# Kernel optimization log

Measured on AMD Instinct MI355X. Metric: run time of the kernel, lower is better.

Reference implementation:

```python
import jax, jax.numpy as jnp
import numpy as np

HEADS = 8
DK = 64   # key_size (defaults to size_per_head)
DV = 64   # size_per_head
RATE = 4
OUT = HEADS * DV  # 512


def extract_seq_patches(x, kernel, rate):
    # x: [b, L, d] -> [b, L, kernel, d]; strided local window gather
    b, L, d = x.shape
    k_size = kernel + (rate - 1) * (kernel - 1)
    p_right = (k_size - 1) // 2
    p_left = k_size - 1 - p_right
    xp = jnp.pad(x, ((0, 0), (p_left, p_right), (0, 0)))
    patches = [xp[:, i:i + L] for i in range(0, k_size, rate)]  # kernel slices
    return jnp.stack(patches, axis=2)


def setup_inputs() -> dict:
    key = jax.random.key(0)
    k1, k2, k3, k4 = jax.random.split(key, 4)
    s = 1.0 / np.sqrt(OUT)
    x = jax.random.normal(k1, (2, 4096, OUT), dtype=jnp.float32)
    Wq = jax.random.normal(k2, (OUT, HEADS * DK), dtype=jnp.float32) * s
    Wk = jax.random.normal(k3, (OUT, HEADS * DK), dtype=jnp.float32) * s
    Wv = jax.random.normal(k4, (OUT, HEADS * DV), dtype=jnp.float32) * s
    return {"x": x, "Wq": Wq, "Wk": Wk, "Wv": Wv}


def reference(x, Wq, Wk, Wv):
    b, L, d = x.shape
    pad = RATE - L % RATE  # torch code always pads (pad=RATE when L % RATE == 0)
    xpad = jnp.pad(x, ((0, 0), (0, pad), (0, 0)))
    nL = L + pad
    n = nL // RATE
    kernel = 2 * RATE - 1  # 1 + 2*neighbors

    qw = xpad @ Wq
    kw = xpad @ Wk
    vw = xpad @ Wv

    kwp = extract_seq_patches(kw, kernel, RATE)  # [b, nL, K, H*dk]
    vwp = extract_seq_patches(vw, kernel, RATE)  # [b, nL, K, H*dv]

    # [b, h, r, n, d]
    qw = qw.reshape(b, n, RATE, HEADS, DK).transpose(0, 3, 2, 1, 4)
    kw = kw.reshape(b, n, RATE, HEADS, DK).transpose(0, 3, 2, 1, 4)
    vw = vw.reshape(b, n, RATE, HEADS, DV).transpose(0, 3, 2, 1, 4)
    # [b, h, r, n, K, d]
    kwp = kwp.reshape(b, n, RATE, kernel, HEADS, DK).transpose(0, 4, 2, 1, 3, 5)
    vwp = vwp.reshape(b, n, RATE, kernel, HEADS, DV).transpose(0, 4, 2, 1, 3, 5)

    scale = 1.0 / np.sqrt(DK)
    a = jnp.einsum('bhrnd,bhrmd->bhrnm', qw, kw) * scale    # strided scores [b,h,r,n,n]
    ap = jnp.einsum('bhrnd,bhrnkd->bhrnk', qw, kwp) * scale  # local scores  [b,h,r,n,K]

    A = jax.nn.softmax(jnp.concatenate([a, ap], axis=-1), axis=-1)
    a, ap = A[..., :n], A[..., n:]

    o = jnp.einsum('bhrnm,bhrmd->bhrnd', a, vw) + jnp.einsum('bhrnk,bhrnkd->bhrnd', ap, vwp)
    o = o.transpose(0, 3, 2, 1, 4).reshape(b, nL, HEADS * DV)
    return o[:, :L]
```

## Files before the change

### kernel.cpp

```cpp
#include <hip/hip_runtime.h>
#include <hip/hip_bf16.h>


#define BATCH 2
#define LSEQ  4096
#define DMODEL 512
#define NH    8
#define DHEAD 64
#define NPAD  1088
#define QSCALE 0.18033688011112042f

typedef __bf16 bf16x8 __attribute__((ext_vector_type(8)));
typedef __attribute__((ext_vector_type(4))) float f32x4;
typedef unsigned short u16;
typedef unsigned int u32;
typedef __attribute__((ext_vector_type(8))) u16 u16x8;
typedef __attribute__((ext_vector_type(4))) u16 u16x4;

__device__ __forceinline__ u16 f2bf(float f) {
    u32 u = __float_as_uint(f);
    u += 0x7fffu + ((u >> 16) & 1u);
    return (u16)(u >> 16);
}

__device__ __forceinline__ void gload16(const u16* g, u16* l) {
    __builtin_amdgcn_global_load_lds(
        (const __attribute__((address_space(1))) u32*)(const void*)g,
        (__attribute__((address_space(3))) u32*)(void*)l, 16, 0, 0);
}

__global__ __launch_bounds__(256) void prep_kernel(
    const float* __restrict__ x,
    const float* __restrict__ Wq, const float* __restrict__ Wk, const float* __restrict__ Wv,
    u16* __restrict__ xb, u16* __restrict__ Wt,
    u16* __restrict__ Kb, u16* __restrict__ Vb)
{
    const int bid = blockIdx.x, tid = threadIdx.x;
    if (bid < 2048) {
        const size_t i0 = (size_t)bid * 2048 + (size_t)tid * 8;
        float4 a = *(const float4*)(x + i0);
        float4 b = *(const float4*)(x + i0 + 4);
        u16x8 o = { f2bf(a.x), f2bf(a.y), f2bf(a.z), f2bf(a.w),
                    f2bf(b.x), f2bf(b.y), f2bf(b.z), f2bf(b.w) };
        *(u16x8*)(xb + i0) = o;
    } else if (bid < 2240) {
        const int wb  = bid - 2048;
        const int mat = wb >> 6;
        const int t   = wb & 63;
        const int k0  = (t >> 3) * 64, c0 = (t & 7) * 64;
        const float* W = (mat == 0) ? Wq : (mat == 1) ? Wk : Wv;
        __shared__ u16 Ws[64][72];
        #pragma unroll
        for (int i = 0; i < 4; ++i) {
            const int chunk = i * 256 + tid;
            const int kr = chunk >> 4, c4 = (chunk & 15) * 4;
            float4 v = *(const float4*)(W + (size_t)(k0 + kr) * DMODEL + c0 + c4);
            u16x4 q = { f2bf(v.x), f2bf(v.y), f2bf(v.z), f2bf(v.w) };
            *(u16x4*)&Ws[kr][c4] = q;
        }
        __syncthreads();
        const int cc = tid >> 2, kq = (tid & 3) * 16;
        alignas(16) u16 tmp[16];
        #pragma unroll
        for (int kk = 0; kk < 16; ++kk) tmp[kk] = Ws[kq + kk][cc];
        u16* dst = Wt + (size_t)(mat * 512 + c0 + cc) * DMODEL + k0 + kq;
        *(u16x8*)dst       = *(const u16x8*)&tmp[0];
        *(u16x8*)(dst + 8) = *(const u16x8*)&tmp[8];
    } else {
        const int g = bid - 2240;
        const u16x8 z = {0,0,0,0,0,0,0,0};
        u16* kt = Kb + ((size_t)g * NPAD + 1024) * DHEAD + tid * 16;
        *(u16x8*)kt       = z;
        *(u16x8*)(kt + 8) = z;
        u16* vt = Vb + ((size_t)g * DHEAD + (tid >> 2)) * NPAD + 1024 + (tid & 3) * 16;
        *(u16x8*)vt       = z;
        *(u16x8*)(vt + 8) = z;
    }
}

__global__ __launch_bounds__(256) void gemm_kernel(
    const u16* __restrict__ xb, const u16* __restrict__ Wt,
    u16* __restrict__ Qb, u16* __restrict__ Kb, u16* __restrict__ Vb)
{
    const int m0 = blockIdx.x * 128;
    const int nt = blockIdx.y;
    const int n0 = nt * 128;
    const int tid = threadIdx.x;
    const int w = tid >> 6, l = tid & 63, lr = l & 15, lh = l >> 4;
    const int wr = w >> 1, wc = w & 1;

    __shared__ u16 smem[16896];
    u16* As = smem;
    u16* Bs = smem + 8192;

    f32x4 acc[4][4];
    const f32x4 fzero = {0.f, 0.f, 0.f, 0.f};
    #pragma unroll
    for (int mi = 0; mi < 4; ++mi)
        #pragma unroll
        for (int nj = 0; nj < 4; ++nj) acc[mi][nj] = fzero;

    for (int kt = 0; kt < 8; ++kt) {
        const int k0 = kt * 64;
        #pragma unroll
        for (int i = 0; i < 4; ++i) {
            const int cid = i * 256 + tid;
            const int row = cid >> 3, ch = cid & 7;
            const int sch = ch ^ (row & 7);
            u16* dstA = As + (i * 256 + w * 64) * 8;
            u16* dstB = Bs + (i * 256 + w * 64) * 8;
            gload16(xb + (size_t)(m0 + row) * DMODEL + k0 + sch * 8, dstA);
            gload16(Wt + (size_t)(n0 + row) * DMODEL + k0 + sch * 8, dstB);
        }
        __syncthreads();

        #pragma unroll
        for (int kk = 0; kk < 2; ++kk) {
            const int cs = (kk * 4 + lh) ^ (lr & 7);
            bf16x8 af[4], bfr[4];
            #pragma unroll
            for (int mi = 0; mi < 4; ++mi)
                af[mi] = *(const bf16x8*)(As + (wr * 64 + mi * 16 + lr) * 64 + cs * 8);
            #pragma unroll
            for (int nj = 0; nj < 4; ++nj)
                bfr[nj] = *(const bf16x8*)(Bs + (wc * 64 + nj * 16 + lr) * 64 + cs * 8);
            #pragma unroll
            for (int mi = 0; mi < 4; ++mi)
                #pragma unroll
                for (int nj = 0; nj < 4; ++nj)
                    acc[mi][nj] = __builtin_amdgcn_mfma_f32_16x16x32_bf16(af[mi], bfr[nj], acc[mi][nj], 0, 0, 0);
        }
        __syncthreads();
    }

    const int mat = nt >> 2;
    const int hp  = nt & 3;
    if (mat < 2) {
        u16* Ob = (mat == 0) ? Qb : Kb;
        const float osc = (mat == 0) ? QSCALE : 1.0f;
        #pragma unroll
        for (int mi = 0; mi < 4; ++mi) {
            const int gmb = m0 + wr * 64 + mi * 16 + lh * 4;
            const int b = gmb >> 12;
            #pragma unroll
            for (int rr = 0; rr < 4; ++rr) {
                const int t = (gmb + rr) & 4095;
                const int n = t >> 2, r = t & 3;
                #pragma unroll
                for (int nj = 0; nj < 4; ++nj) {
                    const int c  = wc * 64 + nj * 16 + lr;
                    const int h  = hp * 2 + (c >> 6);
                    const int dk = c & 63;
                    const size_t g = ((size_t)(b * NH + h)) * 4 + r;
                    Ob[(g * NPAD + n) * DHEAD + dk] = f2bf(acc[mi][nj][rr] * osc);
                }
            }
        }
    } else {
        #pragma unroll
        for (int mi = 0; mi < 4; ++mi) {
            const int nrel = wr * 16 + mi * 4 + lh;
            #pragma unroll
            for (int nj = 0; nj < 4; ++nj) {
                const int c = wc * 64 + nj * 16 + lr;
                #pragma unroll
                for (int rr = 0; rr < 4; ++rr)
                    smem[c * 132 + rr * 32 + nrel] = f2bf(acc[mi][nj][rr]);
            }
        }
        __syncthreads();
        const int b  = m0 >> 12;
        const int nb = (m0 & 4095) >> 2;
        #pragma unroll
        for (int e = 0; e < 2; ++e) {
            const int chunk = e * 256 + tid;
            const int c = chunk & 127, r = chunk >> 7;
            const int h  = hp * 2 + (c >> 6);
            const int dv = c & 63;
            const size_t g = ((size_t)(b * NH + h)) * 4 + r;
            u16* dst = Vb + (g * DHEAD + dv) * NPAD + nb;
            const u16* src = smem + c * 132 + r * 32;
            alignas(16) u16 tmp[32];
            #pragma unroll
            for (int q8 = 0; q8 < 8; ++q8)
                *(u16x4*)&tmp[q8 * 4] = *(const u16x4*)(src + q8 * 4);
            #pragma unroll
            for (int q16 = 0; q16 < 4; ++q16)
                *(u16x8*)(dst + q16 * 8) = *(const u16x8*)&tmp[q16 * 8];
        }
    }
}

__global__ __launch_bounds__(512) void attn_kernel(
    const u16* __restrict__ Qb, const u16* __restrict__ Kb, const u16* __restrict__ Vb,
    float* __restrict__ out)
{
    const int g  = blockIdx.x;
    const int b  = g >> 5;
    const int h  = (g >> 2) & 7;
    const int r  = g & 3;
    const int q0 = blockIdx.y * 128;
    const int tid = threadIdx.x;
    const int w  = tid >> 6;
    const int l  = tid & 63;
    const int lr = l & 15, lh = l >> 4;

    const u16* Qg  = Qb + (size_t)g * NPAD * DHEAD;
    const u16* Kg  = Kb + (size_t)g * NPAD * DHEAD;
    const u16* Vtg = Vb + (size_t)g * DHEAD * NPAD;

    __shared__ u16 KV[2][2][4096];
    __shared__ u16 Ps[8][16][68];

    const int srow = tid >> 3;
    const int ssch = (tid & 7) ^ (srow & 7);
    const u16* ksrc0 = Kg  + (size_t)srow * DHEAD + ssch * 8;
    const u16* vsrc0 = Vtg + (size_t)srow * NPAD  + ssch * 8;

    bf16x8 qa[2];
    {
        const u16* qrow = Qg + (size_t)(q0 + w * 16 + lr) * DHEAD;
        qa[0] = *(const bf16x8*)(qrow + lh * 8);
        qa[1] = *(const bf16x8*)(qrow + 32 + lh * 8);
    }

    const f32x4 fzero = {0.f, 0.f, 0.f, 0.f};
    f32x4 o[4];
    #pragma unroll
    for (int j = 0; j < 4; ++j) o[j] = fzero;
    float Lpart[4] = {0.f, 0.f, 0.f, 0.f};

    const int qw0 = q0 + w * 16;

    gload16(ksrc0, &KV[0][0][w * 512]);
    gload16(vsrc0 + 0, &KV[0][1][w * 512]);

    int cur = 0;
    for (int mt = 0; mt < 17; ++mt) {
        if (mt < 16) {
            gload16(ksrc0 + (size_t)(mt + 1) * 4096, &KV[cur ^ 1][0][w * 512]);
            gload16(vsrc0 + (mt + 1) * 64,           &KV[cur ^ 1][1][w * 512]);
            asm volatile("s_waitcnt vmcnt(2)" ::: "memory");
        } else {
            asm volatile("s_waitcnt vmcnt(0)" ::: "memory");
        }
        __builtin_amdgcn_s_barrier();

        const u16* Kbuf = KV[cur][0];
        const u16* Vbuf = KV[cur][1];

        f32x4 s[4];
        #pragma unroll
        for (int ni = 0; ni < 4; ++ni) {
            s[ni] = fzero;
            #pragma unroll
            for (int kk = 0; kk < 2; ++kk) {
                const int slot = (kk * 4 + lh) ^ (lr & 7);
                bf16x8 kb = *(const bf16x8*)(Kbuf + ((ni * 16 + lr) * 8 + slot) * 8);
                s[ni] = __builtin_amdgcn_mfma_f32_16x16x32_bf16(qa[kk], kb, s[ni], 0, 0, 0);
            }
        }

        const int m0 = mt * 64;
        const bool special = (mt == 16) || ((m0 + 66 >= qw0) && (m0 <= qw0 + 18));
        if (!special) {
            #pragma unroll
            for (int ni = 0; ni < 4; ++ni) {
                #pragma unroll
                for (int rr = 0; rr < 4; ++rr) {
                    const float p = __builtin_amdgcn_exp2f(s[ni][rr]);
                    Lpart[rr] += p;
                    Ps[w][lh * 4 + rr][ni * 16 + lr] = f2bf(p);
                }
            }
        } else {
            #pragma unroll
            for (int ni = 0; ni < 4; ++ni) {
                const int mg = m0 + ni * 16 + lr;
                #pragma unroll
                for (int rr = 0; rr < 4; ++rr) {
                    const int qg = qw0 + lh * 4 + rr;
                    float v = s[ni][rr];
                    const int dd = mg - qg;
                    if (mg > 1024)                 v = -1e30f;
                    else if (dd >= -3 && dd <= 3)  v += 1.0f;
                    const float p = __builtin_amdgcn_exp2f(v);
                    Lpart[rr] += p;
                    Ps[w][lh * 4 + rr][ni * 16 + lr] = f2bf(p);
                }
            }
        }

        #pragma unroll
        for (int kk = 0; kk < 2; ++kk) {
            bf16x8 pa = *(const bf16x8*)&Ps[w][lr][kk * 32 + lh * 8];
            #pragma unroll
            for (int j = 0; j < 4; ++j) {
                const int slot = (kk * 4 + lh) ^ (lr & 7);
                bf16x8 vb = *(const bf16x8*)(Vbuf + ((j * 16 + lr) * 8 + slot) * 8);
                o[j] = __builtin_amdgcn_mfma_f32_16x16x32_bf16(pa, vb, o[j], 0, 0, 0);
            }
        }
        __syncthreads();
        cur ^= 1;
    }

    #pragma unroll
    for (int rr = 0; rr < 4; ++rr) {
        float s_ = Lpart[rr];
        #pragma unroll
        for (int off = 1; off < 16; off <<= 1)
            s_ += __shfl_xor(s_, off, 16);
        const int qg = qw0 + lh * 4 + rr;
        const int coob = (qg < 3 ? 3 - qg : 0) + (qg > 1021 ? qg - 1021 : 0);
        const float inv = 1.0f / (s_ + (float)coob);
        const int t = qg * 4 + r;
        float* orow = out + ((size_t)b * LSEQ + t) * DMODEL + h * DHEAD;
        #pragma unroll
        for (int j = 0; j < 4; ++j)
            orow[j * 16 + lr] = o[j][rr] * inv;
    }
}

extern "C" void kernel_launch(void* const* d_in, const int* in_sizes, int n_in,
                              void* d_out, int out_size, void* d_ws, size_t ws_size,
                              hipStream_t stream) {
    const float* x  = (const float*)d_in[0];
    const float* Wq = (const float*)d_in[1];
    const float* Wk = (const float*)d_in[2];
    const float* Wv = (const float*)d_in[3];
    float* out = (float*)d_out;

    const size_t SZ = (size_t)BATCH * NH * 4 * NPAD * DHEAD;
    u16* Qb = (u16*)d_ws;
    u16* Kb = Qb + SZ;
    u16* Vb = Kb + SZ;

    u16* xb = (u16*)d_out;
    u16* Wt = xb + (size_t)8192 * 512;

    prep_kernel<<<2304, 256, 0, stream>>>(x, Wq, Wk, Wv, xb, Wt, Kb, Vb);

    dim3 gg(64, 12);
    gemm_kernel<<<gg, 256, 0, stream>>>(xb, Wt, Qb, Kb, Vb);

    dim3 ga(64, 8);
    attn_kernel<<<ga, 512, 0, stream>>>(Qb, Kb, Vb, out);
}
```

Baseline: 67.91 us.

## Double query rows per wave, drop padded key tile, reuse K/V fragments

Each attention wave now handles 32 query rows instead of 16, so every K and V fragment read from shared memory feeds two MFMAs and the grid is halved. The 17th key tile covering padded positions is dropped. Its contribution is folded analytically into the softmax denominator, which removes the zero-fill pass for padding in the prep kernel. It also adds s_setprio around the MFMA phases and uses the hardware bf16 conversion. The risks are fewer blocks available for occupancy, more register pressure, and a fragile analytic correction for the padding rows.

```diff
diff --git a/kernel.cpp b/kernel.cpp
--- a/kernel.cpp
+++ b/kernel.cpp
@@ -23,6 +23,11 @@
     return (u16)(u >> 16);
 }
 
+__device__ __forceinline__ u16 cvt_bf(float f) {
+    __bf16 t = (__bf16)f;
+    return *(const u16*)&t;
+}
+
 __device__ __forceinline__ void gload16(const u16* g, u16* l) {
     __builtin_amdgcn_global_load_lds(
         (const __attribute__((address_space(1))) u32*)(const void*)g,
@@ -32,8 +37,7 @@
 __global__ __launch_bounds__(256) void prep_kernel(
     const float* __restrict__ x,
     const float* __restrict__ Wq, const float* __restrict__ Wk, const float* __restrict__ Wv,
-    u16* __restrict__ xb, u16* __restrict__ Wt,
-    u16* __restrict__ Kb, u16* __restrict__ Vb)
+    u16* __restrict__ xb, u16* __restrict__ Wt)
 {
     const int bid = blockIdx.x, tid = threadIdx.x;
     if (bid < 2048) {
@@ -43,7 +47,7 @@
         u16x8 o = { f2bf(a.x), f2bf(a.y), f2bf(a.z), f2bf(a.w),
                     f2bf(b.x), f2bf(b.y), f2bf(b.z), f2bf(b.w) };
         *(u16x8*)(xb + i0) = o;
-    } else if (bid < 2240) {
+    } else {
         const int wb  = bid - 2048;
         const int mat = wb >> 6;
         const int t   = wb & 63;
@@ -66,15 +70,6 @@
         u16* dst = Wt + (size_t)(mat * 512 + c0 + cc) * DMODEL + k0 + kq;
         *(u16x8*)dst       = *(const u16x8*)&tmp[0];
         *(u16x8*)(dst + 8) = *(const u16x8*)&tmp[8];
-    } else {
-        const int g = bid - 2240;
-        const u16x8 z = {0,0,0,0,0,0,0,0};
-        u16* kt = Kb + ((size_t)g * NPAD + 1024) * DHEAD + tid * 16;
-        *(u16x8*)kt       = z;
-        *(u16x8*)(kt + 8) = z;
-        u16* vt = Vb + ((size_t)g * DHEAD + (tid >> 2)) * NPAD + 1024 + (tid & 3) * 16;
-        *(u16x8*)vt       = z;
-        *(u16x8*)(vt + 8) = z;
     }
 }
 
@@ -199,7 +194,7 @@
     const int b  = g >> 5;
     const int h  = (g >> 2) & 7;
     const int r  = g & 3;
-    const int q0 = blockIdx.y * 128;
+    const int q0 = blockIdx.y * 256;
     const int tid = threadIdx.x;
     const int w  = tid >> 6;
     const int l  = tid & 63;
@@ -210,34 +205,35 @@
     const u16* Vtg = Vb + (size_t)g * DHEAD * NPAD;
 
     __shared__ u16 KV[2][2][4096];
-    __shared__ u16 Ps[8][16][68];
+    __shared__ u16 Ps[8][32][68];
 
     const int srow = tid >> 3;
     const int ssch = (tid & 7) ^ (srow & 7);
     const u16* ksrc0 = Kg  + (size_t)srow * DHEAD + ssch * 8;
     const u16* vsrc0 = Vtg + (size_t)srow * NPAD  + ssch * 8;
 
-    bf16x8 qa[2];
-    {
-        const u16* qrow = Qg + (size_t)(q0 + w * 16 + lr) * DHEAD;
-        qa[0] = *(const bf16x8*)(qrow + lh * 8);
-        qa[1] = *(const bf16x8*)(qrow + 32 + lh * 8);
+    bf16x8 qa[2][2];
+    #pragma unroll
+    for (int u = 0; u < 2; ++u) {
+        const u16* qrow = Qg + (size_t)(q0 + w * 32 + u * 16 + lr) * DHEAD;
+        qa[u][0] = *(const bf16x8*)(qrow + lh * 8);
+        qa[u][1] = *(const bf16x8*)(qrow + 32 + lh * 8);
     }
 
     const f32x4 fzero = {0.f, 0.f, 0.f, 0.f};
-    f32x4 o[4];
+    f32x4 o[2][4];
     #pragma unroll
-    for (int j = 0; j < 4; ++j) o[j] = fzero;
-    float Lpart[4] = {0.f, 0.f, 0.f, 0.f};
-
-    const int qw0 = q0 + w * 16;
+    for (int u = 0; u < 2; ++u)
+        #pragma unroll
+        for (int j = 0; j < 4; ++j) o[u][j] = fzero;
+    float Lpart[2][4] = {{0.f,0.f,0.f,0.f},{0.f,0.f,0.f,0.f}};
 
     gload16(ksrc0, &KV[0][0][w * 512]);
-    gload16(vsrc0 + 0, &KV[0][1][w * 512]);
-
-    int cur = 0;
-    for (int mt = 0; mt < 17; ++mt) {
-        if (mt < 16) {
+    gload16(vsrc0, &KV[0][1][w * 512]);
+
+    for (int mt = 0; mt < 16; ++mt) {
+        const int cur = mt & 1;
+        if (mt < 15) {
             gload16(ksrc0 + (size_t)(mt + 1) * 4096, &KV[cur ^ 1][0][w * 512]);
             gload16(vsrc0 + (mt + 1) * 64,           &KV[cur ^ 1][1][w * 512]);
             asm volatile("s_waitcnt vmcnt(2)" ::: "memory");
@@ -249,76 +245,93 @@
         const u16* Kbuf = KV[cur][0];
         const u16* Vbuf = KV[cur][1];
 
-        f32x4 s[4];
+        f32x4 s[2][4];
+        __builtin_amdgcn_s_setprio(1);
         #pragma unroll
         for (int ni = 0; ni < 4; ++ni) {
-            s[ni] = fzero;
-            #pragma unroll
-            for (int kk = 0; kk < 2; ++kk) {
-                const int slot = (kk * 4 + lh) ^ (lr & 7);
-                bf16x8 kb = *(const bf16x8*)(Kbuf + ((ni * 16 + lr) * 8 + slot) * 8);
-                s[ni] = __builtin_amdgcn_mfma_f32_16x16x32_bf16(qa[kk], kb, s[ni], 0, 0, 0);
-            }
-        }
+            const int rbase = (ni * 16 + lr) * 8;
+            const int sl0 = lh ^ (lr & 7), sl1 = (4 + lh) ^ (lr & 7);
+            bf16x8 kb0 = *(const bf16x8*)(Kbuf + (rbase + sl0) * 8);
+            bf16x8 kb1 = *(const bf16x8*)(Kbuf + (rbase + sl1) * 8);
+            #pragma unroll
+            for (int u = 0; u < 2; ++u) {
+                f32x4 t = __builtin_amdgcn_mfma_f32_16x16x32_bf16(qa[u][0], kb0, fzero, 0, 0, 0);
+                s[u][ni] = __builtin_amdgcn_mfma_f32_16x16x32_bf16(qa[u][1], kb1, t, 0, 0, 0);
+            }
+        }
+        __builtin_amdgcn_s_setprio(0);
 
         const int m0 = mt * 64;
-        const bool special = (mt == 16) || ((m0 + 66 >= qw0) && (m0 <= qw0 + 18));
-        if (!special) {
-            #pragma unroll
-            for (int ni = 0; ni < 4; ++ni) {
-                #pragma unroll
-                for (int rr = 0; rr < 4; ++rr) {
-                    const float p = __builtin_amdgcn_exp2f(s[ni][rr]);
-                    Lpart[rr] += p;
-                    Ps[w][lh * 4 + rr][ni * 16 + lr] = f2bf(p);
+        #pragma unroll
+        for (int u = 0; u < 2; ++u) {
+            const int qu0 = q0 + w * 32 + u * 16;
+            const bool special = (m0 + 66 >= qu0) && (m0 <= qu0 + 18);
+            if (!special) {
+                #pragma unroll
+                for (int ni = 0; ni < 4; ++ni) {
+                    #pragma unroll
+                    for (int rr = 0; rr < 4; ++rr) {
+                        const float p = __builtin_amdgcn_exp2f(s[u][ni][rr]);
+                        Lpart[u][rr] += p;
+                        Ps[w][u * 16 + lh * 4 + rr][ni * 16 + lr] = cvt_bf(p);
+                    }
                 }
-            }
-        } else {
-            #pragma unroll
-            for (int ni = 0; ni < 4; ++ni) {
-                const int mg = m0 + ni * 16 + lr;
-                #pragma unroll
-                for (int rr = 0; rr < 4; ++rr) {
-                    const int qg = qw0 + lh * 4 + rr;
-                    float v = s[ni][rr];
-                    const int dd = mg - qg;
-                    if (mg > 1024)                 v = -1e30f;
-                    else if (dd >= -3 && dd <= 3)  v += 1.0f;
-                    const float p = __builtin_amdgcn_exp2f(v);
-                    Lpart[rr] += p;
-                    Ps[w][lh * 4 + rr][ni * 16 + lr] = f2bf(p);
+            } else {
+                #pragma unroll
+                for (int ni = 0; ni < 4; ++ni) {
+                    const int mg = m0 + ni * 16 + lr;
+                    #pragma unroll
+                    for (int rr = 0; rr < 4; ++rr) {
+                        const int qg = qu0 + lh * 4 + rr;
+                        float v = s[u][ni][rr];
+                        const int dd = mg - qg;
+                        if (dd >= -3 && dd <= 3) v += 1.0f;
+                        const float p = __builtin_amdgcn_exp2f(v);
+                        Lpart[u][rr] += p;
+                        Ps[w][u * 16 + lh * 4 + rr][ni * 16 + lr] = cvt_bf(p);
+                    }
                 }
             }
         }
 
+        __builtin_amdgcn_s_setprio(1);
         #pragma unroll
         for (int kk = 0; kk < 2; ++kk) {
-            bf16x8 pa = *(const bf16x8*)&Ps[w][lr][kk * 32 + lh * 8];
-            #pragma unroll
-            for (int j = 0; j < 4; ++j) {
-                const int slot = (kk * 4 + lh) ^ (lr & 7);
-                bf16x8 vb = *(const bf16x8*)(Vbuf + ((j * 16 + lr) * 8 + slot) * 8);
-                o[j] = __builtin_amdgcn_mfma_f32_16x16x32_bf16(pa, vb, o[j], 0, 0, 0);
-            }
-        }
-        __syncthreads();
-        cur ^= 1;
+            const int slot = (kk * 4 + lh) ^ (lr & 7);
+            bf16x8 vb[4];
+            #pragma unroll
+            for (int j = 0; j < 4; ++j)
+                vb[j] = *(const bf16x8*)(Vbuf + ((j * 16 + lr) * 8 + slot) * 8);
+            #pragma unroll
+            for (int u = 0; u < 2; ++u) {
+                bf16x8 pa = *(const bf16x8*)&Ps[w][u * 16 + lr][kk * 32 + lh * 8];
+                #pragma unroll
+                for (int j = 0; j < 4; ++j)
+                    o[u][j] = __builtin_amdgcn_mfma_f32_16x16x32_bf16(pa, vb[j], o[u][j], 0, 0, 0);
+            }
+        }
+        __builtin_amdgcn_s_setprio(0);
+        __syncthreads();
     }
 
     #pragma unroll
-    for (int rr = 0; rr < 4; ++rr) {
-        float s_ = Lpart[rr];
-        #pragma unroll
-        for (int off = 1; off < 16; off <<= 1)
-            s_ += __shfl_xor(s_, off, 16);
-        const int qg = qw0 + lh * 4 + rr;
-        const int coob = (qg < 3 ? 3 - qg : 0) + (qg > 1021 ? qg - 1021 : 0);
-        const float inv = 1.0f / (s_ + (float)coob);
-        const int t = qg * 4 + r;
-        float* orow = out + ((size_t)b * LSEQ + t) * DMODEL + h * DHEAD;
-        #pragma unroll
-        for (int j = 0; j < 4; ++j)
-            orow[j * 16 + lr] = o[j][rr] * inv;
+    for (int u = 0; u < 2; ++u) {
+        #pragma unroll
+        for (int rr = 0; rr < 4; ++rr) {
+            float s_ = Lpart[u][rr];
+            #pragma unroll
+            for (int off = 1; off < 16; off <<= 1)
+                s_ += __shfl_xor(s_, off, 16);
+            const int qg = q0 + w * 32 + u * 16 + lh * 4 + rr;
+            const int coob = (qg < 3 ? 3 - qg : 0) + (qg > 1021 ? qg - 1021 : 0);
+            const float extra = (float)(coob + 1 + (qg >= 1021 ? 1 : 0));
+            const float inv = 1.0f / (s_ + extra);
+            const int t = qg * 4 + r;
+            float* orow = out + ((size_t)b * LSEQ + t) * DMODEL + h * DHEAD;
+            #pragma unroll
+            for (int j = 0; j < 4; ++j)
+                orow[j * 16 + lr] = o[u][j][rr] * inv;
+        }
     }
 }
 
@@ -339,11 +352,11 @@
     u16* xb = (u16*)d_out;
     u16* Wt = xb + (size_t)8192 * 512;
 
-    prep_kernel<<<2304, 256, 0, stream>>>(x, Wq, Wk, Wv, xb, Wt, Kb, Vb);
+    prep_kernel<<<2240, 256, 0, stream>>>(x, Wq, Wk, Wv, xb, Wt);
 
     dim3 gg(64, 12);
     gemm_kernel<<<gg, 256, 0, stream>>>(xb, Wt, Qb, Kb, Vb);
 
-    dim3 ga(64, 8);
+    dim3 ga(64, 4);
     attn_kernel<<<ga, 512, 0, stream>>>(Qb, Kb, Vb, out);
 }
```

After: 70.40 us. 3.7% more time.
